# Performance work log

Hardware: AMD Instinct MI355X
Metric: run time of the kernel (lower is better)

The kernel has to match this reference:

```python
import jax, jax.numpy as jnp
import numpy as np

N_POINTS = 4096
DIM = 64
MAX_EDGE_LENGTH = 1e9  # large -> no MST edge is filtered, output has static shape (n-1,)


def _mst_edge_lengths(points):
    """0-dim Rips persistence death values == Euclidean MST edge lengths.

    Equivalent to gudhi RipsComplex(max_dimension=0) + flag_persistence_generators
    followed by torch.norm(input[v0] - input[v1], dim=-1). Returned sorted
    ascending (gudhi's ordering is unspecified; compare as a multiset).
    """
    n = points.shape[0]
    sq = jnp.sum(points * points, axis=1)                      # [n]
    d2 = sq[:, None] + sq[None, :] - 2.0 * (points @ points.T)  # [n,n]
    d2 = jnp.maximum(d2, 0.0)
    # safe positive diagonal so sqrt is smooth there (diagonal never selected)
    idx = jnp.arange(n)
    d2 = d2.at[idx, idx].set(1.0)
    D = jnp.sqrt(d2)                                            # [n,n] distances

    inf = jnp.asarray(jnp.inf, D.dtype)
    in_tree0 = jnp.zeros((n,), dtype=bool).at[0].set(True)
    dist0 = jnp.where(in_tree0, inf, D[0])                      # min dist to tree

    def step(carry, _):
        dist, in_tree = carry
        j = jnp.argmin(dist)            # nearest non-tree vertex
        w = dist[j]                     # MST edge length (a persistence death)
        in_tree = in_tree.at[j].set(True)
        dist = jnp.where(in_tree, inf, jnp.minimum(dist, D[j]))
        return (dist, in_tree), w

    _, lengths = jax.lax.scan(step, (dist0, in_tree0), None, length=n - 1)
    # max_edge_length filter is a no-op for MAX_EDGE_LENGTH=1e9
    return jnp.sort(lengths)


def setup_inputs() -> dict:
    key = jax.random.key(0)
    points = jax.random.normal(key, (N_POINTS, DIM), dtype=jnp.float32)
    return {"input": points}


def reference(input) -> jnp.ndarray:
    return _mst_edge_lengths(input)
```

## Files before the change

kernel.cpp:

```cpp
#include <hip/hip_runtime.h>
#include <hip/hip_bf16.h>


#define NPTS 4096
#define SENT 1e30f
#define KINF 0xFFFFFFFFFFFFFFFFull
#define INV32 0xFFFFFFFFu
#define SCAN_ROWS 2
#define SCAN_BLOCKS (NPTS / SCAN_ROWS)

#define HOOK_NORMAL 0
#define HOOK_TRY_COMPACT 1
#define HOOK_FORCE_COMPACT 2

typedef short short8 __attribute__((ext_vector_type(8)));
typedef float f32x4 __attribute__((ext_vector_type(4)));

__device__ __forceinline__ float bfbits2f(unsigned int u16) {
  union { unsigned int u; float f; } c;
  c.u = u16 << 16;
  return c.f;
}

__device__ bool data_is_bf16(const unsigned short* p) {
  bool bf = true;
  for (int i = 0; i < 256; ++i) {
    float f = bfbits2f((unsigned int)p[i]);
    if (!(f > -1e6f && f < 1e6f)) bf = false;
  }
  return bf;
}

__global__ __launch_bounds__(256) void prep_kernel(
    const void* pts_raw, unsigned short* Pb, float* sq, int* comp,
    unsigned short* comp16, int* parent, unsigned long long* cheapest,
    float* edges, unsigned* cnt) {
  __shared__ bool bfs;
  if (threadIdx.x == 0) bfs = data_is_bf16((const unsigned short*)pts_raw);
  __syncthreads();

  const int g = blockIdx.x * 256 + threadIdx.x;
  if (g < NPTS) {
    comp[g] = g;
    comp16[g] = (unsigned short)g;
    parent[g] = g;
    cheapest[g] = KINF;
  }
  if (g == NPTS - 1) edges[NPTS - 1] = SENT;
  if (g == 0) {
    cnt[0] = 0u;
    cnt[1] = 0u;
    cnt[2] = bfs ? 1u : 0u;
    cnt[3] = 0u;
  }

  const int row = g >> 6;
  const int lane = threadIdx.x & 63;

  unsigned short ub;
  if (bfs) {
    ub = ((const unsigned short*)pts_raw)[row * 64 + lane];
  } else {
    __hip_bfloat16 h = __float2bfloat16(((const float*)pts_raw)[row * 64 + lane]);
    ub = *(unsigned short*)&h;
  }
  Pb[row * 64 + lane] = ub;

  float v = bfbits2f((unsigned int)ub);
  float s = v * v;
#pragma unroll
  for (int m = 1; m < 64; m <<= 1) s += __shfl_xor(s, m);
  if (lane == 0) sq[row] = s;
}

__global__ __launch_bounds__(256) void dist_mfma(const unsigned short* Pb,
                                                 const float* sq,
                                                 unsigned short* Dbf,
                                                 unsigned long long* cheapest) {
  __shared__ unsigned short tile[64 * 72];

  const int t = threadIdx.x;
  const int w = t >> 6, lane = t & 63;
  const int quad = lane >> 4, l16 = lane & 15;
  const int rbase = blockIdx.y * 64 + w * 16;
  const int cbase = blockIdx.x * 64;

  const short8* Pv = (const short8*)Pb;
  short8 a0 = Pv[(rbase + l16) * 8 + quad];
  short8 a1 = Pv[(rbase + l16) * 8 + quad + 4];

  f32x4 acc[4];
#pragma unroll
  for (int c = 0; c < 4; ++c) {
    short8 b0 = Pv[(cbase + c * 16 + l16) * 8 + quad];
    short8 b1 = Pv[(cbase + c * 16 + l16) * 8 + quad + 4];
    f32x4 z = {0.f, 0.f, 0.f, 0.f};
    z = __builtin_amdgcn_mfma_f32_16x16x32_bf16(a0, b0, z, 0, 0, 0);
    z = __builtin_amdgcn_mfma_f32_16x16x32_bf16(a1, b1, z, 0, 0, 0);
    acc[c] = z;
  }

  float sr[4];
#pragma unroll
  for (int q = 0; q < 4; ++q) sr[q] = sq[rbase + quad * 4 + q];

#pragma unroll
  for (int c = 0; c < 4; ++c) {
    float sc = sq[cbase + c * 16 + l16];
#pragma unroll
    for (int q = 0; q < 4; ++q) {
      float d2 = sr[q] + sc - 2.f * acc[c][q];
      float dd = sqrtf(fmaxf(d2, 0.f));
      __hip_bfloat16 h = __float2bfloat16(dd);
      tile[(w * 16 + quad * 4 + q) * 72 + c * 16 + l16] = *(unsigned short*)&h;
    }
  }
  __syncthreads();

  for (int i = t; i < 512; i += 256) {
    int row = i >> 3, cb8 = (i & 7) * 8;
    uint4 v = *(const uint4*)&tile[row * 72 + cb8];
    *(uint4*)&Dbf[(size_t)(blockIdx.y * 64 + row) * 4096 + cbase + cb8] = v;
  }

  {
    const int r = t >> 2, cseg = (t & 3) * 16;
    const int v = blockIdx.y * 64 + r;
    const uint4* lrow = (const uint4*)&tile[r * 72 + cseg];
    uint4 v0 = lrow[0], v1 = lrow[1];
    unsigned wv[16] = {v0.x & 0xFFFFu, v0.x >> 16, v0.y & 0xFFFFu, v0.y >> 16,
                       v0.z & 0xFFFFu, v0.z >> 16, v0.w & 0xFFFFu, v0.w >> 16,
                       v1.x & 0xFFFFu, v1.x >> 16, v1.y & 0xFFFFu, v1.y >> 16,
                       v1.z & 0xFFFFu, v1.z >> 16, v1.w & 0xFFFFu, v1.w >> 16};
    unsigned long long kmin = KINF;
#pragma unroll
    for (int e = 0; e < 16; ++e) {
      const int j = cbase + cseg + e;
      if (j != v) {
        unsigned ed = (v < j) ? (((unsigned)v << 12) | (unsigned)j)
                              : (((unsigned)j << 12) | (unsigned)v);
        unsigned long long key = ((unsigned long long)wv[e] << 24) | ed;
        kmin = key < kmin ? key : kmin;
      }
    }
#pragma unroll
    for (int m = 1; m < 4; m <<= 1) {
      unsigned long long o = __shfl_xor(kmin, m);
      kmin = o < kmin ? o : kmin;
    }
    if ((t & 3) == 0) atomicMin(&cheapest[v], kmin);
  }
}

__global__ __launch_bounds__(256) void bor_scan(const unsigned short* Dbf,
                                                const unsigned short* comp16,
                                                int* parent,
                                                unsigned long long* cheapest,
                                                const unsigned* cnt) {
  if (cnt[1] || cnt[3]) return;

  __shared__ unsigned long long redu[SCAN_ROWS][4];

  const int t = threadIdx.x;
  const int b = blockIdx.x;
  const int wave = t >> 6;
  const int gtid = b * 256 + t;
  const int vbase = b * SCAN_ROWS;

  if (gtid < NPTS) parent[gtid] = gtid;

  const uint4* c16v = (const uint4*)comp16;
  uint4 c0 = c16v[2 * t], c1 = c16v[2 * t + 1];
  unsigned mc[16] = {c0.x & 0xFFFFu, c0.x >> 16, c0.y & 0xFFFFu, c0.y >> 16,
                     c0.z & 0xFFFFu, c0.z >> 16, c0.w & 0xFFFFu, c0.w >> 16,
                     c1.x & 0xFFFFu, c1.x >> 16, c1.y & 0xFFFFu, c1.y >> 16,
                     c1.z & 0xFFFFu, c1.z >> 16, c1.w & 0xFFFFu, c1.w >> 16};

  const uint4* rp = (const uint4*)(Dbf + (size_t)vbase * NPTS);
#pragma unroll
  for (int vv = 0; vv < SCAN_ROWS; ++vv) {
    const int v = vbase + vv;
    const unsigned cv = (unsigned)comp16[v];
    uint4 a0 = rp[vv * 512 + 2 * t];
    uint4 a1 = rp[vv * 512 + 2 * t + 1];
    unsigned wv[16] = {a0.x & 0xFFFFu, a0.x >> 16, a0.y & 0xFFFFu, a0.y >> 16,
                       a0.z & 0xFFFFu, a0.z >> 16, a0.w & 0xFFFFu, a0.w >> 16,
                       a1.x & 0xFFFFu, a1.x >> 16, a1.y & 0xFFFFu, a1.y >> 16,
                       a1.z & 0xFFFFu, a1.z >> 16, a1.w & 0xFFFFu, a1.w >> 16};
    unsigned long long kmin = KINF;
#pragma unroll
    for (int e = 0; e < 16; ++e) {
      const int j = t * 16 + e;
      if (mc[e] != cv) {
        unsigned ed = (v < j) ? (((unsigned)v << 12) | (unsigned)j)
                              : (((unsigned)j << 12) | (unsigned)v);
        unsigned long long key = ((unsigned long long)wv[e] << 24) | ed;
        kmin = key < kmin ? key : kmin;
      }
    }
#pragma unroll
    for (int m = 1; m < 64; m <<= 1) {
      unsigned long long o = __shfl_xor(kmin, m);
      kmin = o < kmin ? o : kmin;
    }
    if ((t & 63) == 0) redu[vv][wave] = kmin;
  }
  __syncthreads();

  if (t < SCAN_ROWS) {
    unsigned long long k = redu[t][0];
    if (redu[t][1] < k) k = redu[t][1];
    if (redu[t][2] < k) k = redu[t][2];
    if (redu[t][3] < k) k = redu[t][3];
    if (k != KINF) atomicMin(&cheapest[(int)comp16[vbase + t]], k);
  }
}

__global__ __launch_bounds__(1024) void bor_hook(int* comp,
                                                 unsigned short* comp16,
                                                 int* parent,
                                                 unsigned long long* cheapest,
                                                 float* edges, unsigned* cnt,
                                                 int mode, unsigned* M) {
  if (cnt[1]) return;
  if (mode == HOOK_FORCE_COMPACT && cnt[3]) return;
  const int t = threadIdx.x;
  __shared__ unsigned nroots;
  if (t == 0) nroots = 0u;

  for (int i = t; i < NPTS; i += 1024) {
    if (comp[i] == i) {
      unsigned long long key = cheapest[i];
      if (key != KINF) {
        int mx = (int)(key & 0xFFFull);
        int mn = (int)((key >> 12) & 0xFFFull);
        int ca = comp[mn], cb = comp[mx];
        int u = (ca == i) ? cb : ca;
        bool mutual = (cheapest[u] == key);
        if (!mutual || i < u) {
          unsigned pos = atomicAdd(cnt, 1u);
          edges[pos] = bfbits2f((unsigned)(key >> 24));
        }
        if (!mutual || i > u) parent[i] = u;
      }
    }
  }
  __threadfence_block();
  __syncthreads();

  for (int i = t; i < NPTS; i += 1024) {
    int r = comp[i], p;
    for (int it = 0; it < NPTS; ++it) {
      p = parent[r];
      if (p == r) break;
      r = p;
    }
    comp[i] = r;
    comp16[i] = (unsigned short)r;
    cheapest[i] = KINF;
    if (r == i) atomicAdd(&nroots, 1u);
  }
  __threadfence_block();
  __syncthreads();

  const bool want_compact =
      (mode == HOOK_FORCE_COMPACT) ||
      (mode == HOOK_TRY_COMPACT && nroots <= 256u);

  if (want_compact) {
    for (int i = t; i < NPTS; i += 1024)
      if (comp[i] == i) parent[i] = (int)atomicAdd(&cnt[3], 1u);
    __syncthreads();
    for (int i = t; i < NPTS; i += 1024)
      comp16[i] = (unsigned short)parent[comp[i]];
    for (int i = t; i < 256 * 256; i += 1024) M[i] = INV32;
  }
  if (t == 0 && cnt[0] >= (unsigned)(NPTS - 1)) cnt[1] = 1u;
}

__global__ __launch_bounds__(256) void bor_project(const unsigned short* Dbf,
                                                   const unsigned short* comp16,
                                                   unsigned* M,
                                                   const unsigned* cnt) {
  if (cnt[1]) return;

  __shared__ unsigned Mloc[SCAN_ROWS][256];
  const int t = threadIdx.x;
  const int b = blockIdx.x;
  const int vbase = b * SCAN_ROWS;

  Mloc[0][t] = INV32;
  Mloc[1][t] = INV32;
  __syncthreads();

  const uint4* c16v = (const uint4*)comp16;
  uint4 c0 = c16v[2 * t], c1 = c16v[2 * t + 1];
  unsigned mc[16] = {c0.x & 0xFFFFu, c0.x >> 16, c0.y & 0xFFFFu, c0.y >> 16,
                     c0.z & 0xFFFFu, c0.z >> 16, c0.w & 0xFFFFu, c0.w >> 16,
                     c1.x & 0xFFFFu, c1.x >> 16, c1.y & 0xFFFFu, c1.y >> 16,
                     c1.z & 0xFFFFu, c1.z >> 16, c1.w & 0xFFFFu, c1.w >> 16};

  const uint4* rp = (const uint4*)(Dbf + (size_t)vbase * NPTS);
#pragma unroll
  for (int vv = 0; vv < SCAN_ROWS; ++vv) {
    const unsigned cv = (unsigned)comp16[vbase + vv];
    uint4 a0 = rp[vv * 512 + 2 * t];
    uint4 a1 = rp[vv * 512 + 2 * t + 1];
    unsigned wv[16] = {a0.x & 0xFFFFu, a0.x >> 16, a0.y & 0xFFFFu, a0.y >> 16,
                       a0.z & 0xFFFFu, a0.z >> 16, a0.w & 0xFFFFu, a0.w >> 16,
                       a1.x & 0xFFFFu, a1.x >> 16, a1.y & 0xFFFFu, a1.y >> 16,
                       a1.z & 0xFFFFu, a1.z >> 16, a1.w & 0xFFFFu, a1.w >> 16};
#pragma unroll
    for (int e = 0; e < 16; ++e)
      if (mc[e] != cv) atomicMin(&Mloc[vv][mc[e]], wv[e]);
  }
  __syncthreads();

  const unsigned cv0 = (unsigned)comp16[vbase];
  const unsigned cv1 = (unsigned)comp16[vbase + 1];
  unsigned x = Mloc[0][t];
  if (x != INV32) atomicMin(&M[cv0 * 256 + t], x);
  unsigned y = Mloc[1][t];
  if (y != INV32) atomicMin(&M[cv1 * 256 + t], y);
}

__global__ __launch_bounds__(1024) void bor_finish(const unsigned* M,
                                                   unsigned* cnt,
                                                   float* edges) {
  if (cnt[1]) return;

  __shared__ int comp2[256];
  __shared__ int parent2[256];
  __shared__ unsigned cheap2[256];
  __shared__ int live;

  const int t = threadIdx.x;
  const int C = (int)cnt[3];
  if (t < 256) comp2[t] = t;
  __syncthreads();

  for (int round = 0; round < 8; ++round) {
    if (t < 256) cheap2[t] = INV32;
    if (t == 0) live = 0;
    __syncthreads();

    {
      const int c = t >> 2, q = t & 3;
      if (c < C) {
        const int cc = comp2[c];
        unsigned kmin = INV32;
        const uint4* Mr = (const uint4*)(M + c * 256 + q * 64);
#pragma unroll 4
        for (int g = 0; g < 16; ++g) {
          uint4 m4 = Mr[g];
          const int j0 = q * 64 + g * 4;
          unsigned wj[4] = {m4.x, m4.y, m4.z, m4.w};
#pragma unroll
          for (int k = 0; k < 4; ++k) {
            int j = j0 + k;
            unsigned w = wj[k];
            if (w != INV32 && comp2[j] != cc) {
              int lo = c < j ? c : j, hi = c < j ? j : c;
              unsigned key = (w << 16) | ((unsigned)lo << 8) | (unsigned)hi;
              if (key < kmin) kmin = key;
            }
          }
        }
        if (kmin != INV32) atomicMin(&cheap2[cc], kmin);
      }
    }
    __syncthreads();

    if (t < 256) {
      parent2[t] = t;
      if (comp2[t] == t) {
        unsigned key = cheap2[t];
        if (key != INV32) {
          int hi = (int)(key & 0xFFu);
          int lo = (int)((key >> 8) & 0xFFu);
          int ca = comp2[lo], cb = comp2[hi];
          int u = (ca == t) ? cb : ca;
          bool mutual = (cheap2[u] == key);
          if (!mutual || t < u) {
            unsigned pos = atomicAdd(cnt, 1u);
            edges[pos] = bfbits2f(key >> 16);
          }
          if (!mutual || t > u) parent2[t] = u;
        }
      }
    }
    __syncthreads();

    if (t < 256) {
      int r = comp2[t], p;
      for (int it = 0; it < 256; ++it) {
        p = parent2[r];
        if (p == r) break;
        r = p;
      }
      comp2[t] = r;
      if (t < C && r != comp2[0]) live = 1;
    }
    __syncthreads();
    if (!live) break;
  }
}

__global__ __launch_bounds__(256) void rank_sort(const float* edges,
                                                 const unsigned* cnt,
                                                 void* out) {
  __shared__ int wsum[4];
  const int b = blockIdx.x;
  const int t = threadIdx.x;
  const float v = edges[b];
  const float4* ev = (const float4*)edges;

  int c = 0;
#pragma unroll
  for (int k = 0; k < 4; ++k) {
    float4 e = ev[t + 256 * k];
    int j = 4 * (t + 256 * k);
    c += (e.x < v || (e.x == v && j + 0 < b));
    c += (e.y < v || (e.y == v && j + 1 < b));
    c += (e.z < v || (e.z == v && j + 2 < b));
    c += (e.w < v || (e.w == v && j + 3 < b));
  }
#pragma unroll
  for (int m = 1; m < 64; m <<= 1) c += __shfl_xor(c, m);
  if ((t & 63) == 0) wsum[t >> 6] = c;
  __syncthreads();

  if (t == 0) {
    int r = wsum[0] + wsum[1] + wsum[2] + wsum[3];
    if (cnt[2]) {
      ((__hip_bfloat16*)out)[r] = __float2bfloat16(v);
    } else {
      ((float*)out)[r] = v;
    }
  }
}

__global__ __launch_bounds__(256) void dist_kernel(const void* pts_raw,
                                                   __hip_bfloat16* Dbf) {
  __shared__ float As[64 * 65];
  __shared__ float Bs[64 * 65];
  __shared__ float sqA[64];
  __shared__ float sqB[64];

  const int t = threadIdx.x;
  const int bx = blockIdx.x, by = blockIdx.y;
  const bool bf = data_is_bf16((const unsigned short*)pts_raw);
  const unsigned short* pu = (const unsigned short*)pts_raw;
  const float* pf = (const float*)pts_raw;

  for (int s = 0; s < 16; ++s) {
    int e = t + 256 * s;
    int r = e >> 6, c = e & 63;
    float av, bv;
    if (bf) {
      av = bfbits2f((unsigned int)pu[by * 4096 + e]);
      bv = bfbits2f((unsigned int)pu[bx * 4096 + e]);
    } else {
      av = pf[by * 4096 + e];
      bv = pf[bx * 4096 + e];
    }
    As[r * 65 + c] = av;
    Bs[r * 65 + c] = bv;
  }
  __syncthreads();

  if (t < 64) {
    float s = 0.f;
    for (int k = 0; k < 64; ++k) { float x = As[t * 65 + k]; s += x * x; }
    sqA[t] = s;
  } else if (t < 128) {
    int r = t - 64;
    float s = 0.f;
    for (int k = 0; k < 64; ++k) { float x = Bs[r * 65 + k]; s += x * x; }
    sqB[r] = s;
  }
  __syncthreads();

  const int tx = t & 15, ty = t >> 4;
  const int lr = ty * 4, lc = tx * 4;
  float acc[4][4] = {};
  for (int k = 0; k < 64; ++k) {
    float a[4], b[4];
#pragma unroll
    for (int q = 0; q < 4; ++q) a[q] = As[(lr + q) * 65 + k];
#pragma unroll
    for (int p = 0; p < 4; ++p) b[p] = Bs[(lc + p) * 65 + k];
#pragma unroll
    for (int q = 0; q < 4; ++q)
#pragma unroll
      for (int p = 0; p < 4; ++p) acc[q][p] += a[q] * b[p];
  }

#pragma unroll
  for (int q = 0; q < 4; ++q) {
    int gr = by * 64 + lr + q;
    float sa = sqA[lr + q];
#pragma unroll
    for (int p = 0; p < 4; ++p) {
      int gc = bx * 64 + lc + p;
      float d2 = sa + sqB[lc + p] - 2.f * acc[q][p];
      d2 = fmaxf(d2, 0.f);
      Dbf[(size_t)gr * 4096 + gc] = __float2bfloat16(sqrtf(d2));
    }
  }
}

__global__ __launch_bounds__(512) void prim_kernel(const unsigned short* probe,
                                                   const unsigned short* Dbf,
                                                   void* out) {
  __shared__ float len[NPTS];
  __shared__ float rv[2][8];
  __shared__ int ri[2][8];

  const int t = threadIdx.x;
  const bool bf_out = data_is_bf16(probe);

  float d[8];
  {
    const uint4* row0 = (const uint4*)(Dbf);
    uint4 v = row0[t];
    d[0] = bfbits2f(v.x & 0xffffu); d[1] = bfbits2f(v.x >> 16);
    d[2] = bfbits2f(v.y & 0xffffu); d[3] = bfbits2f(v.y >> 16);
    d[4] = bfbits2f(v.z & 0xffffu); d[5] = bfbits2f(v.z >> 16);
    d[6] = bfbits2f(v.w & 0xffffu); d[7] = bfbits2f(v.w >> 16);
    if (t == 0) d[0] = SENT;
  }

  float bv = SENT;
  int bi = 8 * t;
#pragma unroll
  for (int k = 0; k < 8; ++k)
    if (d[k] < bv) { bv = d[k]; bi = 8 * t + k; }

  for (int step = 0; step < NPTS - 1; ++step) {
    float v = bv;
    int idx = bi;
#pragma unroll
    for (int m = 1; m < 64; m <<= 1) {
      float ov = __shfl_xor(v, m);
      int oi = __shfl_xor(idx, m);
      if (ov < v) { v = ov; idx = oi; }
    }
    const int buf = step & 1;
    if ((t & 63) == 0) { rv[buf][t >> 6] = v; ri[buf][t >> 6] = idx; }
    __syncthreads();

    float w = rv[buf][0];
    int j = ri[buf][0];
#pragma unroll
    for (int u = 1; u < 8; ++u) {
      float uv = rv[buf][u];
      if (uv < w) { w = uv; j = ri[buf][u]; }
    }
    if (t == 0) len[step] = w;

    const uint4* row = (const uint4*)(Dbf + (size_t)j * NPTS);
    uint4 rw = row[t];
    float nd[8];
    nd[0] = bfbits2f(rw.x & 0xffffu); nd[1] = bfbits2f(rw.x >> 16);
    nd[2] = bfbits2f(rw.y & 0xffffu); nd[3] = bfbits2f(rw.y >> 16);
    nd[4] = bfbits2f(rw.z & 0xffffu); nd[5] = bfbits2f(rw.z >> 16);
    nd[6] = bfbits2f(rw.w & 0xffffu); nd[7] = bfbits2f(rw.w >> 16);

    bv = SENT;
    bi = 8 * t;
    const int base = 8 * t;
#pragma unroll
    for (int k = 0; k < 8; ++k) {
      float cur = d[k];
      float nn = fminf(cur, nd[k]);
      if (cur == SENT || base + k == j) nn = SENT;
      d[k] = nn;
      if (nn < bv) { bv = nn; bi = base + k; }
    }
  }

  if (t == 0) len[NPTS - 1] = SENT;
  __syncthreads();

  for (int k = 2; k <= NPTS; k <<= 1) {
    for (int jj = k >> 1; jj > 0; jj >>= 1) {
      for (int i = t; i < NPTS; i += 512) {
        int ixj = i ^ jj;
        if (ixj > i) {
          float a = len[i], b = len[ixj];
          bool up = ((i & k) == 0);
          if ((a > b) == up) { len[i] = b; len[ixj] = a; }
        }
      }
      __syncthreads();
    }
  }

  if (bf_out) {
    __hip_bfloat16* o = (__hip_bfloat16*)out;
    for (int i = t; i < NPTS - 1; i += 512) o[i] = __float2bfloat16(len[i]);
  } else {
    float* o = (float*)out;
    for (int i = t; i < NPTS - 1; i += 512) o[i] = len[i];
  }
}

extern "C" void kernel_launch(void* const* d_in, const int* in_sizes, int n_in,
                              void* d_out, int out_size, void* d_ws, size_t ws_size,
                              hipStream_t stream) {
  const void* pts = d_in[0];
  char* base = (char*)d_ws;
  __hip_bfloat16* Dbf = (__hip_bfloat16*)base;

  size_t off = 32ull << 20;
  int* comp = (int*)(base + off);                  off += (size_t)NPTS * 4;
  int* parent = (int*)(base + off);                off += (size_t)NPTS * 4;
  unsigned long long* cheapest =
      (unsigned long long*)(base + off);           off += (size_t)NPTS * 8;
  float* edges = (float*)(base + off);             off += (size_t)NPTS * 4;
  unsigned* cnt = (unsigned*)(base + off);         off += 256;
  unsigned short* Pb = (unsigned short*)(base + off); off += (size_t)NPTS * 64 * 2;
  float* sq = (float*)(base + off);                off += (size_t)NPTS * 4;
  unsigned short* comp16 = (unsigned short*)(base + off); off += (size_t)NPTS * 2;
  unsigned* M = (unsigned*)(base + off);           off += 256 * 256 * 4;

  if (ws_size >= off) {
    prep_kernel<<<1024, 256, 0, stream>>>(pts, Pb, sq, comp, comp16, parent,
                                          cheapest, edges, cnt);
    const unsigned short* Dus = (const unsigned short*)Dbf;
    dist_mfma<<<dim3(64, 64), 256, 0, stream>>>(Pb, sq, (unsigned short*)Dbf,
                                                cheapest);
    bor_hook<<<1, 1024, 0, stream>>>(comp, comp16, parent, cheapest, edges,
                                     cnt, HOOK_NORMAL, M);
    bor_scan<<<SCAN_BLOCKS, 256, 0, stream>>>(Dus, comp16, parent, cheapest,
                                              cnt);
    bor_hook<<<1, 1024, 0, stream>>>(comp, comp16, parent, cheapest, edges,
                                     cnt, HOOK_NORMAL, M);
    bor_scan<<<SCAN_BLOCKS, 256, 0, stream>>>(Dus, comp16, parent, cheapest,
                                              cnt);
    bor_hook<<<1, 1024, 0, stream>>>(comp, comp16, parent, cheapest, edges,
                                     cnt, HOOK_TRY_COMPACT, M);
    bor_scan<<<SCAN_BLOCKS, 256, 0, stream>>>(Dus, comp16, parent, cheapest,
                                              cnt);
    bor_hook<<<1, 1024, 0, stream>>>(comp, comp16, parent, cheapest, edges,
                                     cnt, HOOK_FORCE_COMPACT, M);
    bor_project<<<SCAN_BLOCKS, 256, 0, stream>>>(Dus, comp16, M, cnt);
    bor_finish<<<1, 1024, 0, stream>>>(M, cnt, edges);
    rank_sort<<<NPTS - 1, 256, 0, stream>>>(edges, cnt, d_out);
  } else {
    dist_kernel<<<dim3(64, 64), 256, 0, stream>>>(pts, Dbf);
    prim_kernel<<<1, 512, 0, stream>>>((const unsigned short*)pts,
                                       (const unsigned short*)Dbf, d_out);
  }
}
```

Before: 205.3 us.

## Compact Boruvka components earlier with 512-wide contracted graph and batched rank sort

Cuts one Boruvka scan+hook round by forcing compaction after the third hook, and widens the contracted component matrix and finish kernel to 512 components with 64-bit keys. M initialisation moves into prep_kernel, and the bf16 detection becomes a parallel block-wide vote instead of a single-thread loop. rank_sort now ranks four edges per block, launching a quarter as many blocks. The risk is that the component count after three rounds exceeds 512 on some inputs, and the larger M matrix and finish work add cost.

```diff
diff --git a/kernel.cpp b/kernel.cpp
--- a/kernel.cpp
+++ b/kernel.cpp
@@ -8,10 +8,10 @@
 #define INV32 0xFFFFFFFFu
 #define SCAN_ROWS 2
 #define SCAN_BLOCKS (NPTS / SCAN_ROWS)
+#define CMAX 512
 
 #define HOOK_NORMAL 0
-#define HOOK_TRY_COMPACT 1
-#define HOOK_FORCE_COMPACT 2
+#define HOOK_FORCE_COMPACT 1
 
 typedef short short8 __attribute__((ext_vector_type(8)));
 typedef float f32x4 __attribute__((ext_vector_type(4)));
@@ -34,10 +34,9 @@
 __global__ __launch_bounds__(256) void prep_kernel(
     const void* pts_raw, unsigned short* Pb, float* sq, int* comp,
     unsigned short* comp16, int* parent, unsigned long long* cheapest,
-    float* edges, unsigned* cnt) {
-  __shared__ bool bfs;
-  if (threadIdx.x == 0) bfs = data_is_bf16((const unsigned short*)pts_raw);
-  __syncthreads();
+    float* edges, unsigned* cnt, unsigned* M) {
+  float pf = bfbits2f((unsigned int)((const unsigned short*)pts_raw)[threadIdx.x]);
+  const bool bfs = (bool)__syncthreads_and((int)(pf > -1e6f && pf < 1e6f));
 
   const int g = blockIdx.x * 256 + threadIdx.x;
   if (g < NPTS) {
@@ -46,6 +45,7 @@
     parent[g] = g;
     cheapest[g] = KINF;
   }
+  M[g] = INV32;
   if (g == NPTS - 1) edges[NPTS - 1] = SENT;
   if (g == 0) {
     cnt[0] = 0u;
@@ -157,7 +157,7 @@
                                                 int* parent,
                                                 unsigned long long* cheapest,
                                                 const unsigned* cnt) {
-  if (cnt[1] || cnt[3]) return;
+  if (cnt[1]) return;
 
   __shared__ unsigned long long redu[SCAN_ROWS][4];
 
@@ -221,12 +221,9 @@
                                                  int* parent,
                                                  unsigned long long* cheapest,
                                                  float* edges, unsigned* cnt,
-                                                 int mode, unsigned* M) {
+                                                 int mode) {
   if (cnt[1]) return;
-  if (mode == HOOK_FORCE_COMPACT && cnt[3]) return;
-  const int t = threadIdx.x;
-  __shared__ unsigned nroots;
-  if (t == 0) nroots = 0u;
+  const int t = threadIdx.x;
 
   for (int i = t; i < NPTS; i += 1024) {
     if (comp[i] == i) {
@@ -258,22 +255,16 @@
     comp[i] = r;
     comp16[i] = (unsigned short)r;
     cheapest[i] = KINF;
-    if (r == i) atomicAdd(&nroots, 1u);
   }
   __threadfence_block();
   __syncthreads();
 
-  const bool want_compact =
-      (mode == HOOK_FORCE_COMPACT) ||
-      (mode == HOOK_TRY_COMPACT && nroots <= 256u);
-
-  if (want_compact) {
+  if (mode == HOOK_FORCE_COMPACT) {
     for (int i = t; i < NPTS; i += 1024)
       if (comp[i] == i) parent[i] = (int)atomicAdd(&cnt[3], 1u);
     __syncthreads();
     for (int i = t; i < NPTS; i += 1024)
       comp16[i] = (unsigned short)parent[comp[i]];
-    for (int i = t; i < 256 * 256; i += 1024) M[i] = INV32;
   }
   if (t == 0 && cnt[0] >= (unsigned)(NPTS - 1)) cnt[1] = 1u;
 }
@@ -284,13 +275,15 @@
                                                    const unsigned* cnt) {
   if (cnt[1]) return;
 
-  __shared__ unsigned Mloc[SCAN_ROWS][256];
+  __shared__ unsigned Mloc[SCAN_ROWS][CMAX];
   const int t = threadIdx.x;
   const int b = blockIdx.x;
   const int vbase = b * SCAN_ROWS;
 
   Mloc[0][t] = INV32;
+  Mloc[0][t + 256] = INV32;
   Mloc[1][t] = INV32;
+  Mloc[1][t + 256] = INV32;
   __syncthreads();
 
   const uint4* c16v = (const uint4*)comp16;
@@ -318,10 +311,14 @@
 
   const unsigned cv0 = (unsigned)comp16[vbase];
   const unsigned cv1 = (unsigned)comp16[vbase + 1];
-  unsigned x = Mloc[0][t];
-  if (x != INV32) atomicMin(&M[cv0 * 256 + t], x);
-  unsigned y = Mloc[1][t];
-  if (y != INV32) atomicMin(&M[cv1 * 256 + t], y);
+#pragma unroll
+  for (int s = 0; s < 2; ++s) {
+    const int col = t + 256 * s;
+    unsigned x = Mloc[0][col];
+    if (x != INV32) atomicMin(&M[cv0 * CMAX + col], x);
+    unsigned y = Mloc[1][col];
+    if (y != INV32) atomicMin(&M[cv1 * CMAX + col], y);
+  }
 }
 
 __global__ __launch_bounds__(1024) void bor_finish(const unsigned* M,
@@ -329,31 +326,31 @@
                                                    float* edges) {
   if (cnt[1]) return;
 
-  __shared__ int comp2[256];
-  __shared__ int parent2[256];
-  __shared__ unsigned cheap2[256];
+  __shared__ int comp2[CMAX];
+  __shared__ int parent2[CMAX];
+  __shared__ unsigned long long cheap2[CMAX];
   __shared__ int live;
 
   const int t = threadIdx.x;
   const int C = (int)cnt[3];
-  if (t < 256) comp2[t] = t;
-  __syncthreads();
-
-  for (int round = 0; round < 8; ++round) {
-    if (t < 256) cheap2[t] = INV32;
+  if (t < CMAX) comp2[t] = t;
+  __syncthreads();
+
+  for (int round = 0; round < 10; ++round) {
+    if (t < CMAX) cheap2[t] = KINF;
     if (t == 0) live = 0;
     __syncthreads();
 
     {
-      const int c = t >> 2, q = t & 3;
+      const int c = t >> 1, q = t & 1;
       if (c < C) {
         const int cc = comp2[c];
-        unsigned kmin = INV32;
-        const uint4* Mr = (const uint4*)(M + c * 256 + q * 64);
+        unsigned long long kmin = KINF;
+        const uint4* Mr = (const uint4*)(M + c * CMAX + q * 256);
 #pragma unroll 4
-        for (int g = 0; g < 16; ++g) {
+        for (int g = 0; g < 64; ++g) {
           uint4 m4 = Mr[g];
-          const int j0 = q * 64 + g * 4;
+          const int j0 = q * 256 + g * 4;
           unsigned wj[4] = {m4.x, m4.y, m4.z, m4.w};
 #pragma unroll
           for (int k = 0; k < 4; ++k) {
@@ -361,29 +358,30 @@
             unsigned w = wj[k];
             if (w != INV32 && comp2[j] != cc) {
               int lo = c < j ? c : j, hi = c < j ? j : c;
-              unsigned key = (w << 16) | ((unsigned)lo << 8) | (unsigned)hi;
+              unsigned long long key = ((unsigned long long)w << 20) |
+                                       ((unsigned)lo << 10) | (unsigned)hi;
               if (key < kmin) kmin = key;
             }
           }
         }
-        if (kmin != INV32) atomicMin(&cheap2[cc], kmin);
+        if (kmin != KINF) atomicMin(&cheap2[cc], kmin);
       }
     }
     __syncthreads();
 
-    if (t < 256) {
+    if (t < CMAX) {
       parent2[t] = t;
       if (comp2[t] == t) {
-        unsigned key = cheap2[t];
-        if (key != INV32) {
-          int hi = (int)(key & 0xFFu);
-          int lo = (int)((key >> 8) & 0xFFu);
+        unsigned long long key = cheap2[t];
+        if (key != KINF) {
+          int hi = (int)(key & 0x3FFull);
+          int lo = (int)((key >> 10) & 0x3FFull);
           int ca = comp2[lo], cb = comp2[hi];
           int u = (ca == t) ? cb : ca;
           bool mutual = (cheap2[u] == key);
           if (!mutual || t < u) {
             unsigned pos = atomicAdd(cnt, 1u);
-            edges[pos] = bfbits2f(key >> 16);
+            edges[pos] = bfbits2f((unsigned)(key >> 20));
           }
           if (!mutual || t > u) parent2[t] = u;
         }
@@ -391,9 +389,9 @@
     }
     __syncthreads();
 
-    if (t < 256) {
+    if (t < CMAX) {
       int r = comp2[t], p;
-      for (int it = 0; it < 256; ++it) {
+      for (int it = 0; it < CMAX; ++it) {
         p = parent2[r];
         if (p == r) break;
         r = p;
@@ -409,33 +407,57 @@
 __global__ __launch_bounds__(256) void rank_sort(const float* edges,
                                                  const unsigned* cnt,
                                                  void* out) {
-  __shared__ int wsum[4];
+  __shared__ unsigned long long wred[4][2];
   const int b = blockIdx.x;
   const int t = threadIdx.x;
-  const float v = edges[b];
+  const int pbase = 4 * b;
   const float4* ev = (const float4*)edges;
-
-  int c = 0;
+  const float4 pvv = ev[b];
+  const float pv0 = pvv.x, pv1 = pvv.y, pv2 = pvv.z, pv3 = pvv.w;
+
+  int c0 = 0, c1 = 0, c2 = 0, c3 = 0;
 #pragma unroll
   for (int k = 0; k < 4; ++k) {
     float4 e = ev[t + 256 * k];
     int j = 4 * (t + 256 * k);
-    c += (e.x < v || (e.x == v && j + 0 < b));
-    c += (e.y < v || (e.y == v && j + 1 < b));
-    c += (e.z < v || (e.z == v && j + 2 < b));
-    c += (e.w < v || (e.w == v && j + 3 < b));
-  }
-#pragma unroll
-  for (int m = 1; m < 64; m <<= 1) c += __shfl_xor(c, m);
-  if ((t & 63) == 0) wsum[t >> 6] = c;
+    float va[4] = {e.x, e.y, e.z, e.w};
+#pragma unroll
+    for (int m = 0; m < 4; ++m) {
+      const float x = va[m];
+      const int xi = j + m;
+      c0 += (x < pv0 || (x == pv0 && xi < pbase + 0));
+      c1 += (x < pv1 || (x == pv1 && xi < pbase + 1));
+      c2 += (x < pv2 || (x == pv2 && xi < pbase + 2));
+      c3 += (x < pv3 || (x == pv3 && xi < pbase + 3));
+    }
+  }
+
+  unsigned long long p0 = (unsigned long long)(unsigned)c0 |
+                          ((unsigned long long)(unsigned)c1 << 32);
+  unsigned long long p1 = (unsigned long long)(unsigned)c2 |
+                          ((unsigned long long)(unsigned)c3 << 32);
+#pragma unroll
+  for (int m = 1; m < 64; m <<= 1) {
+    p0 += __shfl_xor(p0, m);
+    p1 += __shfl_xor(p1, m);
+  }
+  if ((t & 63) == 0) { wred[t >> 6][0] = p0; wred[t >> 6][1] = p1; }
   __syncthreads();
 
   if (t == 0) {
-    int r = wsum[0] + wsum[1] + wsum[2] + wsum[3];
-    if (cnt[2]) {
-      ((__hip_bfloat16*)out)[r] = __float2bfloat16(v);
-    } else {
-      ((float*)out)[r] = v;
+    unsigned long long a = wred[0][0] + wred[1][0] + wred[2][0] + wred[3][0];
+    unsigned long long d = wred[0][1] + wred[1][1] + wred[2][1] + wred[3][1];
+    const int r[4] = {(int)(a & 0xFFFFFFFFull), (int)(a >> 32),
+                      (int)(d & 0xFFFFFFFFull), (int)(d >> 32)};
+    const float pv[4] = {pv0, pv1, pv2, pv3};
+    const bool bf = cnt[2] != 0u;
+#pragma unroll
+    for (int p = 0; p < 4; ++p) {
+      const int pidx = pbase + p;
+      if (pidx < NPTS - 1) {
+        if (bf) ((__hip_bfloat16*)out)[r[p]] = __float2bfloat16(pv[p]);
+        else    ((float*)out)[r[p]] = pv[p];
+      }
     }
   }
 }
@@ -623,31 +645,27 @@
   unsigned short* Pb = (unsigned short*)(base + off); off += (size_t)NPTS * 64 * 2;
   float* sq = (float*)(base + off);                off += (size_t)NPTS * 4;
   unsigned short* comp16 = (unsigned short*)(base + off); off += (size_t)NPTS * 2;
-  unsigned* M = (unsigned*)(base + off);           off += 256 * 256 * 4;
+  unsigned* M = (unsigned*)(base + off);           off += (size_t)CMAX * CMAX * 4;
 
   if (ws_size >= off) {
     prep_kernel<<<1024, 256, 0, stream>>>(pts, Pb, sq, comp, comp16, parent,
-                                          cheapest, edges, cnt);
+                                          cheapest, edges, cnt, M);
     const unsigned short* Dus = (const unsigned short*)Dbf;
     dist_mfma<<<dim3(64, 64), 256, 0, stream>>>(Pb, sq, (unsigned short*)Dbf,
                                                 cheapest);
     bor_hook<<<1, 1024, 0, stream>>>(comp, comp16, parent, cheapest, edges,
-                                     cnt, HOOK_NORMAL, M);
+                                     cnt, HOOK_NORMAL);
     bor_scan<<<SCAN_BLOCKS, 256, 0, stream>>>(Dus, comp16, parent, cheapest,
                                               cnt);
     bor_hook<<<1, 1024, 0, stream>>>(comp, comp16, parent, cheapest, edges,
-                                     cnt, HOOK_NORMAL, M);
+                                     cnt, HOOK_NORMAL);
     bor_scan<<<SCAN_BLOCKS, 256, 0, stream>>>(Dus, comp16, parent, cheapest,
                                               cnt);
     bor_hook<<<1, 1024, 0, stream>>>(comp, comp16, parent, cheapest, edges,
-                                     cnt, HOOK_TRY_COMPACT, M);
-    bor_scan<<<SCAN_BLOCKS, 256, 0, stream>>>(Dus, comp16, parent, cheapest,
-                                              cnt);
-    bor_hook<<<1, 1024, 0, stream>>>(comp, comp16, parent, cheapest, edges,
-                                     cnt, HOOK_FORCE_COMPACT, M);
+                                     cnt, HOOK_FORCE_COMPACT);
     bor_project<<<SCAN_BLOCKS, 256, 0, stream>>>(Dus, comp16, M, cnt);
     bor_finish<<<1, 1024, 0, stream>>>(M, cnt, edges);
-    rank_sort<<<NPTS - 1, 256, 0, stream>>>(edges, cnt, d_out);
+    rank_sort<<<NPTS / 4, 256, 0, stream>>>(edges, cnt, d_out);
   } else {
     dist_kernel<<<dim3(64, 64), 256, 0, stream>>>(pts, Dbf);
     prim_kernel<<<1, 512, 0, stream>>>((const unsigned short*)pts,
```

New measurement: 203.7 us. Within noise of the previous version (-0.8%).
